# Performance work log

Hardware: AMD Instinct MI355X
Metric: run time of the kernel (lower is better)

## Reference

```python
import jax, jax.numpy as jnp
import numpy as np

B, C, F = 8, 2048, 128


def setup_inputs() -> dict:
    key = jax.random.key(0)
    ks = jax.random.split(key, 13)
    features = jax.random.normal(ks[0], (B, C, F), dtype=jnp.float32)
    # sparse-ish boolean adjacency masks over operations
    pred_mask = jax.random.uniform(ks[1], (B, C, C)) < 0.05
    succ_mask = jax.random.uniform(ks[2], (B, C, C)) < 0.05
    same_type_mask = jax.random.uniform(ks[3], (B, C, C)) < 0.10

    def linear(k, fan_in, fan_out):
        kw, kb = jax.random.split(k)
        bound = 1.0 / np.sqrt(fan_in)
        W = jax.random.uniform(kw, (fan_in, fan_out), minval=-bound, maxval=bound, dtype=jnp.float32)
        b = jax.random.uniform(kb, (fan_out,), minval=-bound, maxval=bound, dtype=jnp.float32)
        return W, b

    W_enc, b_enc = linear(ks[4], F, 4 * F)
    W_space, b_space = linear(ks[5], 3 * F, F)
    W_same, b_same = linear(ks[6], 2 * F, F)
    W_mix, b_mix = linear(ks[7], 2 * F, F)
    return {
        "features": features,
        "pred_mask": pred_mask,
        "succ_mask": succ_mask,
        "same_type_mask": same_type_mask,
        "W_enc": W_enc, "b_enc": b_enc,
        "W_space": W_space, "b_space": b_space,
        "W_same": W_same, "b_same": b_same,
        "W_mix": W_mix, "b_mix": b_mix,
    }


def reference(features, pred_mask, succ_mask, same_type_mask,
              W_enc, b_enc, W_space, b_space, W_same, b_same, W_mix, b_mix):
    # encoder: [B,C,F] -> [B,C,4F], split into origin + 3 message features
    enc = features @ W_enc + b_enc
    origin, e_pred, e_succ, e_same = jnp.split(enc, 4, axis=-1)

    def masked_mean(mask, e):
        # original builds (B,C,C,F) broadcast product then sums over 'other';
        # mathematically this is mask @ e with a clamped-degree divisor.
        m = mask.astype(e.dtype)                         # [B,C,C]
        deg = jnp.maximum(m.sum(-1, keepdims=True), 1.0)  # [B,C,1]
        return jnp.einsum('bij,bjf->bif', m, e) / deg

    pred_f = masked_mean(pred_mask, e_pred)
    succ_f = masked_mean(succ_mask, e_succ)
    same_f = masked_mean(same_type_mask, e_same)

    space_mixed = jnp.concatenate([pred_f, origin, succ_f], axis=-1) @ W_space + b_space
    same_mixed = jnp.concatenate([origin, same_f], axis=-1) @ W_same + b_same
    return jnp.concatenate([space_mixed, same_mixed], axis=-1) @ W_mix + b_mix
```

## Files before the change

kernel.cpp:

```cpp
#include <hip/hip_runtime.h>
#include <stdint.h>

typedef unsigned int uint;
typedef unsigned short ushort;
typedef unsigned char uchar;
typedef __attribute__((ext_vector_type(8))) short bf16x8;
typedef __attribute__((ext_vector_type(4))) float f32x4;

__device__ __forceinline__ ushort f2bf(float f) {
  uint u = __builtin_bit_cast(uint, f);
  return (ushort)((u + 0x7FFFu + ((u >> 16) & 1u)) >> 16);
}

__global__ __launch_bounds__(256) void k_detect(
    const uint* __restrict__ mp, const uint* __restrict__ ms,
    const uint* __restrict__ mt, int* __restrict__ esz) {
  int bid = blockIdx.x;
  const uint* m = (bid < 64) ? mp : (bid < 128) ? ms : mt;
  uint v = m[(size_t)(bid & 63) * 65521 + threadIdx.x];
  if (!(v == 0u || v == 1u || v == 0x3F800000u)) atomicAnd(esz, 0);
}

__global__ __launch_bounds__(256) void k_pack(
    const void* __restrict__ mp, const void* __restrict__ ms,
    const void* __restrict__ mt, uint* __restrict__ bm,
    float* __restrict__ inv, float* __restrict__ ind,
    const int* __restrict__ esz_p) {
  const int gid = blockIdx.x * 4 + (threadIdx.x >> 6);
  const int lane = threadIdx.x & 63;
  const int mid = gid >> 14;
  const int row = gid & 16383;
  const void* mask = (mid == 0) ? mp : (mid == 1) ? ms : mt;
  const bool is4 = (*esz_p != 0);
  uint w = 0;
  if (is4) {
    const uint* p = (const uint*)mask + (size_t)row * 2048 + lane * 32;
    uint4 v[8];
#pragma unroll
    for (int q = 0; q < 8; ++q) v[q] = *(const uint4*)(p + q * 4);
#pragma unroll
    for (int q = 0; q < 8; ++q) {
      w |= (v[q].x != 0u ? 1u : 0u) << (q * 4 + 0);
      w |= (v[q].y != 0u ? 1u : 0u) << (q * 4 + 1);
      w |= (v[q].z != 0u ? 1u : 0u) << (q * 4 + 2);
      w |= (v[q].w != 0u ? 1u : 0u) << (q * 4 + 3);
    }
  } else {
    const uchar* p = (const uchar*)mask + (size_t)row * 2048 + lane * 32;
    uint4 v0 = *(const uint4*)p;
    uint4 v1 = *(const uint4*)(p + 16);
    uint arr[8] = {v0.x, v0.y, v0.z, v0.w, v1.x, v1.y, v1.z, v1.w};
#pragma unroll
    for (int q = 0; q < 8; ++q)
#pragma unroll
      for (int j = 0; j < 4; ++j)
        w |= (((arr[q] >> (j * 8)) & 0xFFu) ? 1u : 0u) << (q * 4 + j);
  }
  bm[(size_t)gid * 64 + lane] = w;
  int c = __popc(w);
#pragma unroll
  for (int off = 1; off < 64; off <<= 1) c += __shfl_xor(c, off, 64);
  if (lane == 0) {
    inv[gid] = 1.0f / (float)(c > 0 ? c : 1);
    ind[gid] = (c > 0) ? 1.0f : 0.0f;
  }
}

__global__ __launch_bounds__(256) void k_fuse1(
    const float* __restrict__ Ws, const float* __restrict__ Wsame,
    const float* __restrict__ Wm, float* __restrict__ T1, float* __restrict__ T2) {
  int idx = blockIdx.x * 256 + threadIdx.x;
  if (idx >= 81920) return;
  int r = idx >> 7, n = idx & 127;
  float s = 0.f;
  if (r < 384) {
    for (int c = 0; c < 128; ++c) s += Ws[r * 128 + c] * Wm[c * 128 + n];
    T1[r * 128 + n] = s;
  } else {
    int rr = r - 384;
    for (int c = 0; c < 128; ++c) s += Wsame[rr * 128 + c] * Wm[(128 + c) * 128 + n];
    T2[rr * 128 + n] = s;
  }
}

__global__ __launch_bounds__(256) void k_fuse2(
    const float* __restrict__ We, const float* __restrict__ be,
    const float* __restrict__ bs, const float* __restrict__ bsame,
    const float* __restrict__ bm_, const float* __restrict__ Wm,
    const float* __restrict__ T1, const float* __restrict__ T2,
    ushort* __restrict__ UT, float* __restrict__ cvec) {
  int idx = blockIdx.x * 256 + threadIdx.x;
  if (idx < 65536) {
    int y = idx >> 14, n = (idx >> 7) & 127, k = idx & 127;
    float s = 0.f;
    if (y == 0)
      for (int m = 0; m < 128; ++m)
        s += We[k * 512 + m] * (T1[(128 + m) * 128 + n] + T2[m * 128 + n]);
    else if (y == 1)
      for (int m = 0; m < 128; ++m) s += We[k * 512 + 128 + m] * T1[m * 128 + n];
    else if (y == 2)
      for (int m = 0; m < 128; ++m) s += We[k * 512 + 256 + m] * T1[(256 + m) * 128 + n];
    else
      for (int m = 0; m < 128; ++m) s += We[k * 512 + 384 + m] * T2[(128 + m) * 128 + n];
    UT[((size_t)y * 128 + n) * 128 + k] = f2bf(s);
  } else if (idx < 66048) {
    int cid = idx - 65536, cv = cid >> 7, n = cid & 127;
    float s = 0.f;
    if (cv == 0) {
      for (int m = 0; m < 128; ++m)
        s += be[m] * (T1[(128 + m) * 128 + n] + T2[m * 128 + n]);
      for (int c = 0; c < 128; ++c) s += bs[c] * Wm[c * 128 + n];
      for (int c = 0; c < 128; ++c) s += bsame[c] * Wm[(128 + c) * 128 + n];
      s += bm_[n];
    } else if (cv == 1) {
      for (int m = 0; m < 128; ++m) s += be[128 + m] * T1[m * 128 + n];
    } else if (cv == 2) {
      for (int m = 0; m < 128; ++m) s += be[256 + m] * T1[(256 + m) * 128 + n];
    } else {
      for (int m = 0; m < 128; ++m) s += be[384 + m] * T2[(128 + m) * 128 + n];
    }
    cvec[cv * 128 + n] = s;
  }
}

__global__ __launch_bounds__(256) void k_enc(
    const float* __restrict__ feat, const ushort* __restrict__ UT,
    const float* __restrict__ cvec, float* __restrict__ out,
    ushort* __restrict__ eT0, ushort* __restrict__ eT1, ushort* __restrict__ eT2) {
  __shared__ ushort As[64 * 72];
  __shared__ ushort Bs[128 * 72];
  __shared__ ushort stage[8192];
  const int t = threadIdx.x;
  const int gm0 = blockIdx.x * 64;
  const int y = blockIdx.y;
  const int lane = t & 63, wave = t >> 6;
  const int m0w = (wave >> 1) * 32, n0w = (wave & 1) * 64;
  const int quad = lane >> 4, lr = lane & 15;
  const int am = t >> 2, aq = t & 3;
  const int bn = t >> 1, bh = t & 1;
  f32x4 acc[2][4] = {};
  for (int k0 = 0; k0 < 128; k0 += 64) {
    const float* asrc = feat + (size_t)(gm0 + am) * 128 + k0 + aq * 16;
    float4 f0 = *(const float4*)asrc;
    float4 f1 = *(const float4*)(asrc + 4);
    float4 f2 = *(const float4*)(asrc + 8);
    float4 f3 = *(const float4*)(asrc + 12);
    ushort h[16];
    h[0] = f2bf(f0.x); h[1] = f2bf(f0.y); h[2] = f2bf(f0.z); h[3] = f2bf(f0.w);
    h[4] = f2bf(f1.x); h[5] = f2bf(f1.y); h[6] = f2bf(f1.z); h[7] = f2bf(f1.w);
    h[8] = f2bf(f2.x); h[9] = f2bf(f2.y); h[10] = f2bf(f2.z); h[11] = f2bf(f2.w);
    h[12] = f2bf(f3.x); h[13] = f2bf(f3.y); h[14] = f2bf(f3.z); h[15] = f2bf(f3.w);
    const ushort* bsrc = UT + ((size_t)y * 128 + bn) * 128 + k0 + bh * 32;
    bf16x8 bv0 = *(const bf16x8*)bsrc;
    bf16x8 bv1 = *(const bf16x8*)(bsrc + 8);
    bf16x8 bv2 = *(const bf16x8*)(bsrc + 16);
    bf16x8 bv3 = *(const bf16x8*)(bsrc + 24);
    *(bf16x8*)&As[am * 72 + aq * 16] = *(bf16x8*)&h[0];
    *(bf16x8*)&As[am * 72 + aq * 16 + 8] = *(bf16x8*)&h[8];
    *(bf16x8*)&Bs[bn * 72 + bh * 32] = bv0;
    *(bf16x8*)&Bs[bn * 72 + bh * 32 + 8] = bv1;
    *(bf16x8*)&Bs[bn * 72 + bh * 32 + 16] = bv2;
    *(bf16x8*)&Bs[bn * 72 + bh * 32 + 24] = bv3;
    __syncthreads();
#pragma unroll
    for (int kc = 0; kc < 2; ++kc) {
      bf16x8 a[2], b[4];
#pragma unroll
      for (int i = 0; i < 2; ++i)
        a[i] = *(const bf16x8*)&As[(m0w + i * 16 + lr) * 72 + kc * 32 + quad * 8];
#pragma unroll
      for (int j = 0; j < 4; ++j)
        b[j] = *(const bf16x8*)&Bs[(n0w + j * 16 + lr) * 72 + kc * 32 + quad * 8];
#pragma unroll
      for (int i = 0; i < 2; ++i)
#pragma unroll
        for (int j = 0; j < 4; ++j)
          acc[i][j] = __builtin_amdgcn_mfma_f32_16x16x32_bf16(a[i], b[j], acc[i][j], 0, 0, 0);
    }
    __syncthreads();
  }
  if (y == 0) {
#pragma unroll
    for (int i = 0; i < 2; ++i)
#pragma unroll
      for (int j = 0; j < 4; ++j)
#pragma unroll
        for (int r = 0; r < 4; ++r) {
          int m = gm0 + m0w + i * 16 + quad * 4 + r;
          int n = n0w + j * 16 + lr;
          out[(size_t)m * 128 + n] = acc[i][j][r] + cvec[n];
        }
  } else {
#pragma unroll
    for (int i = 0; i < 2; ++i)
#pragma unroll
      for (int j = 0; j < 4; ++j)
#pragma unroll
        for (int r = 0; r < 4; ++r) {
          int rl = m0w + i * 16 + quad * 4 + r;
          int n = n0w + j * 16 + lr;
          int kc = rl >> 5, qd = (rl >> 3) & 3, e = rl & 7;
          stage[((((n >> 4) * 2 + kc) * 4 + qd) * 16 + (n & 15)) * 8 + e] =
              f2bf(acc[i][j][r]);
        }
    __syncthreads();
    ushort* eT = (y == 1) ? eT0 : (y == 2) ? eT1 : eT2;
    ushort* dst = eT + ((size_t)(gm0 >> 11) * 32 + ((gm0 >> 6) & 31)) * 8192 + t * 32;
    const ushort* src = stage + t * 32;
#pragma unroll
    for (int p = 0; p < 4; ++p)
      *(bf16x8*)(dst + p * 8) = *(const bf16x8*)(src + p * 8);
  }
}

__global__ __launch_bounds__(256, 3) void k_mm(
    const uint* __restrict__ bm, const ushort* __restrict__ eT0,
    const ushort* __restrict__ eT1, const ushort* __restrict__ eT2,
    const float* __restrict__ inv, const float* __restrict__ ind,
    const float* __restrict__ cvec, float* __restrict__ P0,
    float* __restrict__ P1, float* __restrict__ P2) {
  __shared__ uint sbm[64][68];
  const int t = threadIdx.x;
  const int id = blockIdx.x;
  const int xcd = id & 7, q = id >> 3;
  const int mtile = q & 31, gg = xcd * 3 + (q >> 5);
  const int b = gg & 7, mid = gg >> 3;
  const ushort* eT = (mid == 0) ? eT0 : (mid == 1) ? eT1 : eT2;
  float* Pm = (mid == 0) ? P0 : (mid == 1) ? P1 : P2;
  const float* cm = cvec + (mid + 1) * 128;
  const size_t rowbase = (size_t)b * 2048 + mtile * 64;
  const uint* bmbase = bm + ((size_t)mid * 16384 + rowbase) * 64;
  {
    int r = t >> 2, c0 = (t & 3) * 16;
    const uint* src = bmbase + (size_t)r * 64 + c0;
    uint4 v0 = *(const uint4*)src;
    uint4 v1 = *(const uint4*)(src + 4);
    uint4 v2 = *(const uint4*)(src + 8);
    uint4 v3 = *(const uint4*)(src + 12);
    *(uint4*)&sbm[r][c0] = v0;
    *(uint4*)&sbm[r][c0 + 4] = v1;
    *(uint4*)&sbm[r][c0 + 8] = v2;
    *(uint4*)&sbm[r][c0 + 12] = v3;
  }
  const int lane = t & 63, wave = t >> 6;
  const int m0w = (wave >> 1) * 32, n0w = (wave & 1) * 64;
  const int quad = lane >> 4, lr = lane & 15;
  const int jb = n0w >> 4;
  const int r0l = m0w + lr, r1l = r0l + 16;
  const ushort* bbase = eT + (size_t)b * 32 * 8192 + quad * 128 + lr * 8;
  f32x4 acc[2][4] = {};
  bf16x8 pb0[4], pb1[4];
#pragma unroll
  for (int j = 0; j < 4; ++j) {
    pb0[j] = *(const bf16x8*)(bbase + (jb + j) * 1024);
    pb1[j] = *(const bf16x8*)(bbase + 512 + (jb + j) * 1024);
  }
  __syncthreads();

#define MM_STEP(IT, PB)                                                       \
  do {                                                                        \
    const int it_ = (IT);                                                     \
    const uint w0 = sbm[r0l][it_];                                            \
    const uint w1 = sbm[r1l][it_];                                            \
    union { bf16x8 v; uint u[4]; } a0, a1;                                    \
    const uint s0 = w0 >> (quad * 8), s1 = w1 >> (quad * 8);                  \
    _Pragma("unroll")                                                         \
    for (int p = 0; p < 4; ++p) {                                             \
      a0.u[p] = (((s0 >> (2 * p)) & 1u) ? 0x3F80u : 0u) |                     \
                (((s0 >> (2 * p)) & 2u) ? 0x3F800000u : 0u);                  \
      a1.u[p] = (((s1 >> (2 * p)) & 1u) ? 0x3F80u : 0u) |                     \
                (((s1 >> (2 * p)) & 2u) ? 0x3F800000u : 0u);                  \
    }                                                                         \
    _Pragma("unroll")                                                         \
    for (int j = 0; j < 4; ++j) {                                             \
      acc[0][j] = __builtin_amdgcn_mfma_f32_16x16x32_bf16(a0.v, PB[j],        \
                                                          acc[0][j], 0, 0, 0);\
      acc[1][j] = __builtin_amdgcn_mfma_f32_16x16x32_bf16(a1.v, PB[j],        \
                                                          acc[1][j], 0, 0, 0);\
    }                                                                         \
    int itn_ = it_ + 2;                                                       \
    if (itn_ > 63) itn_ = 63;                                                 \
    const ushort* bp_ = bbase + (itn_ >> 1) * 8192 + (itn_ & 1) * 512;        \
    _Pragma("unroll")                                                         \
    for (int j = 0; j < 4; ++j)                                               \
      PB[j] = *(const bf16x8*)(bp_ + (jb + j) * 1024);                        \
  } while (0)

  for (int it2 = 0; it2 < 32; ++it2) {
    MM_STEP(2 * it2, pb0);
    MM_STEP(2 * it2 + 1, pb1);
  }
#undef MM_STEP

  float cmv[4];
#pragma unroll
  for (int j = 0; j < 4; ++j) cmv[j] = cm[n0w + j * 16 + lr];
#pragma unroll
  for (int i = 0; i < 2; ++i)
#pragma unroll
    for (int r = 0; r < 4; ++r) {
      const int ml = m0w + i * 16 + quad * 4 + r;
      const size_t row = rowbase + ml;
      const float iv = inv[(size_t)mid * 16384 + row];
      const float id_ = ind[(size_t)mid * 16384 + row];
#pragma unroll
      for (int j = 0; j < 4; ++j) {
        const int n = n0w + j * 16 + lr;
        Pm[row * 128 + n] = acc[i][j][r] * iv + id_ * cmv[j];
      }
    }
}

__global__ __launch_bounds__(256) void k_add(
    float4* __restrict__ out, const float4* __restrict__ P0,
    const float4* __restrict__ P1, const float4* __restrict__ P2) {
  const int i = blockIdx.x * 256 + threadIdx.x;
  float4 o = out[i];
  const float4 a = P0[i], b = P1[i], c = P2[i];
  o.x += a.x + b.x + c.x;
  o.y += a.y + b.y + c.y;
  o.z += a.z + b.z + c.z;
  o.w += a.w + b.w + c.w;
  out[i] = o;
}

extern "C" void kernel_launch(void* const* d_in, const int* in_sizes, int n_in,
                              void* d_out, int out_size, void* d_ws,
                              size_t ws_size, hipStream_t stream) {
  const float* features = (const float*)d_in[0];
  const void* pred = d_in[1];
  const void* succ = d_in[2];
  const void* same = d_in[3];
  const float* W_enc = (const float*)d_in[4];
  const float* b_enc = (const float*)d_in[5];
  const float* W_space = (const float*)d_in[6];
  const float* b_space = (const float*)d_in[7];
  const float* W_same = (const float*)d_in[8];
  const float* b_same = (const float*)d_in[9];
  const float* W_mix = (const float*)d_in[10];
  const float* b_mix = (const float*)d_in[11];
  float* out = (float*)d_out;

  char* wsb = (char*)d_ws;
  ushort* UT = (ushort*)wsb;
  float* cvec = (float*)(wsb + 131072);
  float* T1 = (float*)(wsb + 133120);
  float* T2 = (float*)(wsb + 329728);
  ushort* eT0 = (ushort*)(wsb + 460800);
  ushort* eT1 = (ushort*)(wsb + 460800 + 4194304);
  ushort* eT2 = (ushort*)(wsb + 460800 + 8388608);
  uint* bm = (uint*)(wsb + 13043712);
  float* inv = (float*)(wsb + 25626624);
  float* ind = (float*)(wsb + 25823232);
  float* P0 = (float*)(wsb + 26019840);
  float* P1 = (float*)(wsb + 26019840 + 8388608);
  float* P2 = (float*)(wsb + 26019840 + 16777216);
  int* esz = (int*)(wsb + 51185664);

  hipMemsetAsync(esz, 1, 4, stream);
  k_detect<<<192, 256, 0, stream>>>((const uint*)pred, (const uint*)succ,
                                    (const uint*)same, esz);
  k_pack<<<12288, 256, 0, stream>>>(pred, succ, same, bm, inv, ind, esz);
  k_fuse1<<<320, 256, 0, stream>>>(W_space, W_same, W_mix, T1, T2);
  k_fuse2<<<258, 256, 0, stream>>>(W_enc, b_enc, b_space, b_same, b_mix, W_mix,
                                   T1, T2, UT, cvec);
  k_enc<<<dim3(256, 4), 256, 0, stream>>>(features, UT, cvec, out, eT0, eT1, eT2);
  k_mm<<<768, 256, 0, stream>>>(bm, eT0, eT1, eT2, inv, ind, cvec, P0, P1, P2);
  k_add<<<2048, 256, 0, stream>>>((float4*)out, (const float4*)P0,
                                  (const float4*)P1, (const float4*)P2);
}
```

Baseline: 456.4 us.

## Coalesce mask packing with ballots and fuse encoder output slices per block

The mask pack kernel now reads each row with fully coalesced 16-byte loads across the wave and builds bit words with wave ballots, and the degree comes from ballot popcounts instead of a shuffle reduction. The encoder kernel loads the feature tile once into LDS and loops over all four output slices, reading pre-swizzled MFMA-fragment weights straight from global memory. It also changes the packed bit ordering and the eT layout to match. This cuts redundant feature reads and strided mask loads, at the cost of more global loads of the weight fragments and fewer encoder blocks.

After: 458.4 us. Within noise of the previous version (+0.4%).

```diff
diff --git a/kernel.cpp b/kernel.cpp
--- a/kernel.cpp
+++ b/kernel.cpp
@@ -2,6 +2,7 @@
 #include <stdint.h>
 
 typedef unsigned int uint;
+typedef unsigned long long ull;
 typedef unsigned short ushort;
 typedef unsigned char uchar;
 typedef __attribute__((ext_vector_type(8))) short bf16x8;
@@ -11,6 +12,7 @@
   uint u = __builtin_bit_cast(uint, f);
   return (ushort)((u + 0x7FFFu + ((u >> 16) & 1u)) >> 16);
 }
+
 
 __global__ __launch_bounds__(256) void k_detect(
     const uint* __restrict__ mp, const uint* __restrict__ ms,
@@ -32,38 +34,53 @@
   const int row = gid & 16383;
   const void* mask = (mid == 0) ? mp : (mid == 1) ? ms : mt;
   const bool is4 = (*esz_p != 0);
-  uint w = 0;
+  uint myword = 0;
+  int cnt = 0;
   if (is4) {
-    const uint* p = (const uint*)mask + (size_t)row * 2048 + lane * 32;
-    uint4 v[8];
-#pragma unroll
-    for (int q = 0; q < 8; ++q) v[q] = *(const uint4*)(p + q * 4);
+    const uint* base = (const uint*)mask + (size_t)row * 2048;
+    const int qsel = lane >> 3;
+    const int e0 = (lane >> 1) & 1, e1 = (lane >> 2) & 1;
+    const int hs = (lane & 1) * 32;
 #pragma unroll
     for (int q = 0; q < 8; ++q) {
-      w |= (v[q].x != 0u ? 1u : 0u) << (q * 4 + 0);
-      w |= (v[q].y != 0u ? 1u : 0u) << (q * 4 + 1);
-      w |= (v[q].z != 0u ? 1u : 0u) << (q * 4 + 2);
-      w |= (v[q].w != 0u ? 1u : 0u) << (q * 4 + 3);
+      uint4 v = *(const uint4*)(base + q * 256 + lane * 4);
+      ull b0 = __ballot(v.x != 0u);
+      ull b1 = __ballot(v.y != 0u);
+      ull b2 = __ballot(v.z != 0u);
+      ull b3 = __ballot(v.w != 0u);
+      cnt += __popcll(b0) + __popcll(b1) + __popcll(b2) + __popcll(b3);
+      ull s0 = e0 ? b1 : b0;
+      ull s1 = e0 ? b3 : b2;
+      ull sel = e1 ? s1 : s0;
+      if (qsel == q) myword = (uint)(sel >> hs);
+    }
+    if (lane == 0) {
+      inv[gid] = 1.0f / (float)(cnt > 0 ? cnt : 1);
+      ind[gid] = (cnt > 0) ? 1.0f : 0.0f;
     }
   } else {
-    const uchar* p = (const uchar*)mask + (size_t)row * 2048 + lane * 32;
-    uint4 v0 = *(const uint4*)p;
-    uint4 v1 = *(const uint4*)(p + 16);
-    uint arr[8] = {v0.x, v0.y, v0.z, v0.w, v1.x, v1.y, v1.z, v1.w};
-#pragma unroll
-    for (int q = 0; q < 8; ++q)
-#pragma unroll
-      for (int j = 0; j < 4; ++j)
-        w |= (((arr[q] >> (j * 8)) & 0xFFu) ? 1u : 0u) << (q * 4 + j);
-  }
-  bm[(size_t)gid * 64 + lane] = w;
-  int c = __popc(w);
-#pragma unroll
-  for (int off = 1; off < 64; off <<= 1) c += __shfl_xor(c, off, 64);
-  if (lane == 0) {
-    inv[gid] = 1.0f / (float)(c > 0 ? c : 1);
-    ind[gid] = (c > 0) ? 1.0f : 0.0f;
-  }
+    const uchar* base = (const uchar*)mask + (size_t)row * 2048 +
+                        (lane >> 3) * 256 + (lane & 1) * 128;
+    const int e = (lane >> 1) & 3;
+#pragma unroll
+    for (int p = 0; p < 8; ++p) {
+      uint4 v = *(const uint4*)(base + p * 16);
+      uint a[4] = {v.x, v.y, v.z, v.w};
+#pragma unroll
+      for (int x = 0; x < 4; ++x) {
+        uint bit = (((a[x] >> (8 * e)) & 0xFFu) != 0u) ? 1u : 0u;
+        myword |= bit << (p * 4 + x);
+      }
+    }
+    int c = __popc(myword);
+#pragma unroll
+    for (int off = 1; off < 64; off <<= 1) c += __shfl_xor(c, off, 64);
+    if (lane == 0) {
+      inv[gid] = 1.0f / (float)(c > 0 ? c : 1);
+      ind[gid] = (c > 0) ? 1.0f : 0.0f;
+    }
+  }
+  bm[(size_t)gid * 64 + lane] = myword;
 }
 
 __global__ __launch_bounds__(256) void k_fuse1(
@@ -88,7 +105,7 @@
     const float* __restrict__ bs, const float* __restrict__ bsame,
     const float* __restrict__ bm_, const float* __restrict__ Wm,
     const float* __restrict__ T1, const float* __restrict__ T2,
-    ushort* __restrict__ UT, float* __restrict__ cvec) {
+    ushort* __restrict__ UTf, float* __restrict__ cvec) {
   int idx = blockIdx.x * 256 + threadIdx.x;
   if (idx < 65536) {
     int y = idx >> 14, n = (idx >> 7) & 127, k = idx & 127;
@@ -102,7 +119,9 @@
       for (int m = 0; m < 128; ++m) s += We[k * 512 + 256 + m] * T1[(256 + m) * 128 + n];
     else
       for (int m = 0; m < 128; ++m) s += We[k * 512 + 384 + m] * T2[(128 + m) * 128 + n];
-    UT[((size_t)y * 128 + n) * 128 + k] = f2bf(s);
+    int kb = k >> 6, rl = k & 63;
+    UTf[(size_t)y * 16384 + kb * 8192 + (n >> 4) * 1024 + (rl >> 5) * 512 +
+        ((rl >> 3) & 3) * 128 + (n & 15) * 8 + (rl & 7)] = f2bf(s);
   } else if (idx < 66048) {
     int cid = idx - 65536, cv = cid >> 7, n = cid & 127;
     float s = 0.f;
@@ -124,92 +143,87 @@
 }
 
 __global__ __launch_bounds__(256) void k_enc(
-    const float* __restrict__ feat, const ushort* __restrict__ UT,
+    const float* __restrict__ feat, const ushort* __restrict__ UTf,
     const float* __restrict__ cvec, float* __restrict__ out,
     ushort* __restrict__ eT0, ushort* __restrict__ eT1, ushort* __restrict__ eT2) {
-  __shared__ ushort As[64 * 72];
-  __shared__ ushort Bs[128 * 72];
+  __shared__ ushort As[64 * 136];
   __shared__ ushort stage[8192];
   const int t = threadIdx.x;
   const int gm0 = blockIdx.x * 64;
-  const int y = blockIdx.y;
+  const int b = gm0 >> 11, q = (gm0 >> 8) & 7, d = (gm0 >> 6) & 3;
   const int lane = t & 63, wave = t >> 6;
   const int m0w = (wave >> 1) * 32, n0w = (wave & 1) * 64;
   const int quad = lane >> 4, lr = lane & 15;
-  const int am = t >> 2, aq = t & 3;
-  const int bn = t >> 1, bh = t & 1;
-  f32x4 acc[2][4] = {};
-  for (int k0 = 0; k0 < 128; k0 += 64) {
-    const float* asrc = feat + (size_t)(gm0 + am) * 128 + k0 + aq * 16;
-    float4 f0 = *(const float4*)asrc;
-    float4 f1 = *(const float4*)(asrc + 4);
-    float4 f2 = *(const float4*)(asrc + 8);
-    float4 f3 = *(const float4*)(asrc + 12);
-    ushort h[16];
-    h[0] = f2bf(f0.x); h[1] = f2bf(f0.y); h[2] = f2bf(f0.z); h[3] = f2bf(f0.w);
-    h[4] = f2bf(f1.x); h[5] = f2bf(f1.y); h[6] = f2bf(f1.z); h[7] = f2bf(f1.w);
-    h[8] = f2bf(f2.x); h[9] = f2bf(f2.y); h[10] = f2bf(f2.z); h[11] = f2bf(f2.w);
-    h[12] = f2bf(f3.x); h[13] = f2bf(f3.y); h[14] = f2bf(f3.z); h[15] = f2bf(f3.w);
-    const ushort* bsrc = UT + ((size_t)y * 128 + bn) * 128 + k0 + bh * 32;
-    bf16x8 bv0 = *(const bf16x8*)bsrc;
-    bf16x8 bv1 = *(const bf16x8*)(bsrc + 8);
-    bf16x8 bv2 = *(const bf16x8*)(bsrc + 16);
-    bf16x8 bv3 = *(const bf16x8*)(bsrc + 24);
-    *(bf16x8*)&As[am * 72 + aq * 16] = *(bf16x8*)&h[0];
-    *(bf16x8*)&As[am * 72 + aq * 16 + 8] = *(bf16x8*)&h[8];
-    *(bf16x8*)&Bs[bn * 72 + bh * 32] = bv0;
-    *(bf16x8*)&Bs[bn * 72 + bh * 32 + 8] = bv1;
-    *(bf16x8*)&Bs[bn * 72 + bh * 32 + 16] = bv2;
-    *(bf16x8*)&Bs[bn * 72 + bh * 32 + 24] = bv3;
-    __syncthreads();
-#pragma unroll
-    for (int kc = 0; kc < 2; ++kc) {
-      bf16x8 a[2], b[4];
+  const int jb = n0w >> 4;
+  {
+    const float4* src = (const float4*)(feat + (size_t)gm0 * 128);
+#pragma unroll
+    for (int p = 0; p < 8; ++p) {
+      float4 f = src[p * 256 + t];
+      int idx = p * 1024 + t * 4;
+      int row = idx >> 7, col = idx & 127;
+      ushort4 h4;
+      h4.x = f2bf(f.x); h4.y = f2bf(f.y); h4.z = f2bf(f.z); h4.w = f2bf(f.w);
+      *(ushort4*)&As[row * 136 + col] = h4;
+    }
+  }
+  __syncthreads();
+
+  for (int y = 0; y < 4; ++y) {
+    f32x4 acc[2][4] = {};
+    const ushort* By = UTf + (size_t)y * 16384;
+#pragma unroll
+    for (int kc = 0; kc < 4; ++kc) {
+      bf16x8 a0 = *(const bf16x8*)&As[(m0w + lr) * 136 + kc * 32 + quad * 8];
+      bf16x8 a1 = *(const bf16x8*)&As[(m0w + 16 + lr) * 136 + kc * 32 + quad * 8];
+      const ushort* bp = By + (kc >> 1) * 8192 + (kc & 1) * 512 + quad * 128 + lr * 8;
+      bf16x8 b0 = *(const bf16x8*)(bp + (jb + 0) * 1024);
+      bf16x8 b1 = *(const bf16x8*)(bp + (jb + 1) * 1024);
+      bf16x8 b2 = *(const bf16x8*)(bp + (jb + 2) * 1024);
+      bf16x8 b3 = *(const bf16x8*)(bp + (jb + 3) * 1024);
+      acc[0][0] = __builtin_amdgcn_mfma_f32_16x16x32_bf16(a0, b0, acc[0][0], 0, 0, 0);
+      acc[0][1] = __builtin_amdgcn_mfma_f32_16x16x32_bf16(a0, b1, acc[0][1], 0, 0, 0);
+      acc[0][2] = __builtin_amdgcn_mfma_f32_16x16x32_bf16(a0, b2, acc[0][2], 0, 0, 0);
+      acc[0][3] = __builtin_amdgcn_mfma_f32_16x16x32_bf16(a0, b3, acc[0][3], 0, 0, 0);
+      acc[1][0] = __builtin_amdgcn_mfma_f32_16x16x32_bf16(a1, b0, acc[1][0], 0, 0, 0);
+      acc[1][1] = __builtin_amdgcn_mfma_f32_16x16x32_bf16(a1, b1, acc[1][1], 0, 0, 0);
+      acc[1][2] = __builtin_amdgcn_mfma_f32_16x16x32_bf16(a1, b2, acc[1][2], 0, 0, 0);
+      acc[1][3] = __builtin_amdgcn_mfma_f32_16x16x32_bf16(a1, b3, acc[1][3], 0, 0, 0);
+    }
+    if (y == 0) {
 #pragma unroll
       for (int i = 0; i < 2; ++i)
-        a[i] = *(const bf16x8*)&As[(m0w + i * 16 + lr) * 72 + kc * 32 + quad * 8];
-#pragma unroll
-      for (int j = 0; j < 4; ++j)
-        b[j] = *(const bf16x8*)&Bs[(n0w + j * 16 + lr) * 72 + kc * 32 + quad * 8];
+#pragma unroll
+        for (int j = 0; j < 4; ++j)
+#pragma unroll
+          for (int r = 0; r < 4; ++r) {
+            int m = gm0 + m0w + i * 16 + quad * 4 + r;
+            int n = n0w + j * 16 + lr;
+            out[(size_t)m * 128 + n] = acc[i][j][r] + cvec[n];
+          }
+    } else {
+      __syncthreads();
 #pragma unroll
       for (int i = 0; i < 2; ++i)
 #pragma unroll
         for (int j = 0; j < 4; ++j)
-          acc[i][j] = __builtin_amdgcn_mfma_f32_16x16x32_bf16(a[i], b[j], acc[i][j], 0, 0, 0);
-    }
-    __syncthreads();
-  }
-  if (y == 0) {
-#pragma unroll
-    for (int i = 0; i < 2; ++i)
-#pragma unroll
-      for (int j = 0; j < 4; ++j)
-#pragma unroll
-        for (int r = 0; r < 4; ++r) {
-          int m = gm0 + m0w + i * 16 + quad * 4 + r;
-          int n = n0w + j * 16 + lr;
-          out[(size_t)m * 128 + n] = acc[i][j][r] + cvec[n];
-        }
-  } else {
-#pragma unroll
-    for (int i = 0; i < 2; ++i)
-#pragma unroll
-      for (int j = 0; j < 4; ++j)
-#pragma unroll
-        for (int r = 0; r < 4; ++r) {
-          int rl = m0w + i * 16 + quad * 4 + r;
-          int n = n0w + j * 16 + lr;
-          int kc = rl >> 5, qd = (rl >> 3) & 3, e = rl & 7;
-          stage[((((n >> 4) * 2 + kc) * 4 + qd) * 16 + (n & 15)) * 8 + e] =
-              f2bf(acc[i][j][r]);
-        }
-    __syncthreads();
-    ushort* eT = (y == 1) ? eT0 : (y == 2) ? eT1 : eT2;
-    ushort* dst = eT + ((size_t)(gm0 >> 11) * 32 + ((gm0 >> 6) & 31)) * 8192 + t * 32;
-    const ushort* src = stage + t * 32;
-#pragma unroll
-    for (int p = 0; p < 4; ++p)
-      *(bf16x8*)(dst + p * 8) = *(const bf16x8*)(src + p * 8);
+#pragma unroll
+          for (int r = 0; r < 4; ++r) {
+            int ml = m0w + i * 16 + quad * 4 + r;
+            int n = n0w + j * 16 + lr;
+            stage[(ml & 3) * 2048 + (n >> 4) * 256 + ((ml >> 5) & 1) * 128 +
+                  (n & 15) * 8 + ((ml >> 2) & 7)] = f2bf(acc[i][j][r]);
+          }
+      __syncthreads();
+      ushort* eTy = (y == 1) ? eT0 : (y == 2) ? eT1 : eT2;
+      const int e_t = t >> 6, n2 = (t >> 3) & 7, tt = t & 7;
+      ushort* dst = eTy + ((size_t)(b * 32 + q * 4 + e_t)) * 8192 + n2 * 1024 +
+                    d * 256 + tt * 32;
+      const ushort* src = stage + e_t * 2048 + n2 * 256 + tt * 32;
+#pragma unroll
+      for (int p = 0; p < 4; ++p)
+        *(bf16x8*)(dst + p * 8) = *(const bf16x8*)(src + p * 8);
+    }
   }
 }
 
@@ -342,7 +356,7 @@
   float* out = (float*)d_out;
 
   char* wsb = (char*)d_ws;
-  ushort* UT = (ushort*)wsb;
+  ushort* UTf = (ushort*)wsb;
   float* cvec = (float*)(wsb + 131072);
   float* T1 = (float*)(wsb + 133120);
   float* T2 = (float*)(wsb + 329728);
@@ -363,8 +377,8 @@
   k_pack<<<12288, 256, 0, stream>>>(pred, succ, same, bm, inv, ind, esz);
   k_fuse1<<<320, 256, 0, stream>>>(W_space, W_same, W_mix, T1, T2);
   k_fuse2<<<258, 256, 0, stream>>>(W_enc, b_enc, b_space, b_same, b_mix, W_mix,
-                                   T1, T2, UT, cvec);
-  k_enc<<<dim3(256, 4), 256, 0, stream>>>(features, UT, cvec, out, eT0, eT1, eT2);
+                                   T1, T2, UTf, cvec);
+  k_enc<<<256, 256, 0, stream>>>(features, UTf, cvec, out, eT0, eT1, eT2);
   k_mm<<<768, 256, 0, stream>>>(bm, eT0, eT1, eT2, inv, ind, cvec, P0, P1, P2);
   k_add<<<2048, 256, 0, stream>>>((float4*)out, (const float4*)P0,
                                   (const float4*)P1, (const float4*)P2);
```
